# Optimization experiments

Measured on AMD Instinct MI355X. Metric: run time of the kernel, lower is better.

## Reference

```python
import jax, jax.numpy as jnp
import numpy as np

B, L, HID, H = 4, 1024, 1024, 16
D = HID // H  # 64

def setup_inputs() -> dict:
    key = jax.random.key(0)
    ks = jax.random.split(key, 9)
    s = 0.02
    return {
        'query_states': jax.random.normal(ks[0], (B, L, HID), jnp.float32),
        'key_states':   jax.random.normal(ks[1], (B, L, HID), jnp.float32),
        'value_states': jax.random.normal(ks[2], (B, L, HID), jnp.float32),
        'Wq': jax.random.normal(ks[3], (HID, HID), jnp.float32) * s,
        'bq': jnp.zeros((HID,), jnp.float32),
        'Wk': jax.random.normal(ks[4], (HID, HID), jnp.float32) * s,
        'bk': jnp.zeros((HID,), jnp.float32),
        'Wv': jax.random.normal(ks[5], (HID, HID), jnp.float32) * s,
        'bv': jnp.zeros((HID,), jnp.float32),
        'Wo': jax.random.normal(ks[6], (HID, HID), jnp.float32) * s,
        'bo': jnp.zeros((HID,), jnp.float32),
        'rel_pos_enc': jax.random.normal(ks[7], (2 * L - 1, D), jnp.float32),
    }

def _split_heads(x):
    # [B,L,HID] -> [B,H,L,D]
    return x.reshape(B, L, H, D).transpose(0, 2, 1, 3)

def reference(query_states, key_states, value_states, Wq, bq, Wk, bk, Wv, bv, Wo, bo, rel_pos_enc):
    q = _split_heads(query_states @ Wq + bq)  # [B,H,L,D]
    k = _split_heads(key_states @ Wk + bk)
    v = _split_heads(value_states @ Wv + bv)
    scores = jnp.einsum('bhld,bhrd->bhlr', q, k)
    # relative position bias
    pos = jnp.arange(L)
    distance = pos[:, None] - pos[None, :] + L - 1          # [L,L] in [0, 2L-2]
    pos_emb = rel_pos_enc[distance]                          # [L,L,D]
    scores = scores + jnp.einsum('bhld,lrd->bhlr', q, pos_emb)
    scores = scores / jnp.sqrt(jnp.asarray(D, scores.dtype))
    probs = jax.nn.softmax(scores, axis=-1)                  # dropout p=0 (eval)
    ctx = jnp.einsum('bhlr,bhrd->bhld', probs, v)
    ctx = ctx.transpose(0, 2, 1, 3).reshape(B, L, HID)
    out = ctx @ Wo + bo
    return (out, probs)
```

## Files before the change

### kernel.cpp

```cpp
#include <hip/hip_runtime.h>

typedef __bf16 bf16_t;
typedef bf16_t bf16x8 __attribute__((ext_vector_type(8)));
typedef bf16_t bf16x4 __attribute__((ext_vector_type(4)));
typedef float f32x16 __attribute__((ext_vector_type(16)));
typedef float f32x4v __attribute__((ext_vector_type(4)));
typedef unsigned int u32;

#define DEVI __device__ __forceinline__

DEVI f32x16 zero16() {
  f32x16 z;
#pragma unroll
  for (int i = 0; i < 16; ++i) z[i] = 0.0f;
  return z;
}

DEVI void gload16(const bf16_t* g, const unsigned short* l) {
  __builtin_amdgcn_global_load_lds(
      (const __attribute__((address_space(1))) u32*)g,
      (__attribute__((address_space(3))) u32*)l, 16, 0, 0);
}

union U16B { bf16x8 v; uint4 u; unsigned short s[8]; };
union U4B  { bf16_t h[4]; uint2 u; };

__global__ __launch_bounds__(256) void prep_kernel(
    const float* __restrict__ W0, const float* __restrict__ W1,
    const float* __restrict__ W2, const float* __restrict__ W3,
    bf16_t* __restrict__ T0, bf16_t* __restrict__ T1,
    bf16_t* __restrict__ T2, bf16_t* __restrict__ T3,
    const float* __restrict__ relE, bf16_t* __restrict__ Eb) {
  __shared__ float T[64][65];
  const int bid = blockIdx.x;
  const int tid = threadIdx.x;
  if (bid < 1024) {
    const int sel = bid >> 8;
    const float* W = sel == 0 ? W0 : sel == 1 ? W1 : sel == 2 ? W2 : W3;
    bf16_t* Wt = sel == 0 ? T0 : sel == 1 ? T1 : sel == 2 ? T2 : T3;
    const int bx = bid & 255;
    const int tx = bx & 15, ty = bx >> 4;
    const int k0 = ty * 64, n0 = tx * 64;
    {
      const int r = tid >> 4, c4 = (tid & 15) * 4;
#pragma unroll
      for (int rr = 0; rr < 64; rr += 16) {
        float4 v = *reinterpret_cast<const float4*>(&W[(size_t)(k0 + r + rr) * 1024 + n0 + c4]);
        T[r + rr][c4 + 0] = v.x; T[r + rr][c4 + 1] = v.y;
        T[r + rr][c4 + 2] = v.z; T[r + rr][c4 + 3] = v.w;
      }
    }
    __syncthreads();
    {
      const int r = tid >> 3, c8 = (tid & 7) * 8;
#pragma unroll
      for (int rr = 0; rr < 64; rr += 32) {
        U16B p;
#pragma unroll
        for (int i = 0; i < 8; ++i) p.v[i] = (bf16_t)T[c8 + i][r + rr];
        *reinterpret_cast<uint4*>(&Wt[(size_t)(n0 + r + rr) * 1024 + k0 + c8]) = p.u;
      }
    }
  } else {
    const int q = (bid - 1024) * 256 + tid;
    U4B p;
    if (q < 32752) {
      float4 v = *reinterpret_cast<const float4*>(&relE[(size_t)q * 4]);
      p.h[0] = (bf16_t)v.x; p.h[1] = (bf16_t)v.y; p.h[2] = (bf16_t)v.z; p.h[3] = (bf16_t)v.w;
    } else {
      p.h[0] = p.h[1] = p.h[2] = p.h[3] = (bf16_t)0.0f;
    }
    *reinterpret_cast<uint2*>(&Eb[(size_t)q * 4]) = p.u;
  }
}

#define ROWMAP(reg) (((reg) & 3) + 8 * ((reg) >> 2) + 4 * hi)

__global__ __launch_bounds__(512, 2) void gemm_qkv_kernel(
    const float* __restrict__ X0, const float* __restrict__ X1,
    const float* __restrict__ X2, const bf16_t* __restrict__ W0,
    const bf16_t* __restrict__ W1, const bf16_t* __restrict__ W2,
    const float* __restrict__ b0, const float* __restrict__ b1,
    const float* __restrict__ b2, bf16_t* __restrict__ O0,
    bf16_t* __restrict__ O1, bf16_t* __restrict__ O2) {
  __shared__ __align__(16) unsigned short As[2][256][64];
  __shared__ __align__(16) unsigned short Bs[2][256][64];
  const int f = blockIdx.x;
  const int fp = (f & 7) * 24 + (f >> 3);
  const int op = fp >> 6;
  const int r = fp & 63;
  const float* Xp = op == 0 ? X0 : op == 1 ? X1 : X2;
  const bf16_t* Wt = op == 0 ? W0 : op == 1 ? W1 : W2;
  const float* bias = op == 0 ? b0 : op == 1 ? b1 : b2;
  bf16_t* Out = op == 0 ? O0 : op == 1 ? O1 : O2;
  const int m0 = (r >> 2) * 256, n0 = (r & 3) * 256;
  const int tid = threadIdx.x;
  const int lane = tid & 63, wave = tid >> 6;
  const int hi = lane >> 5, ln = lane & 31;
  const int wr = wave >> 2, wc = wave & 3;
  const int srow = lane >> 3, scol = lane & 7;

  f32x16 acc[4][2];
#pragma unroll
  for (int rt = 0; rt < 4; ++rt) { acc[rt][0] = zero16(); acc[rt][1] = zero16(); }

  float4 fA[4][2];

#define ALOADR(kt)                                                                  \
  {                                                                                 \
    _Pragma("unroll")                                                               \
    for (int j = 0; j < 4; ++j) {                                                   \
      const int row = wave * 32 + j * 8 + srow;                                     \
      const float* src = &Xp[(size_t)(m0 + row) * 1024 + (kt) * 64 + scol * 8];     \
      fA[j][0] = *reinterpret_cast<const float4*>(src);                             \
      fA[j][1] = *reinterpret_cast<const float4*>(src + 4);                         \
    }                                                                               \
  }

#define ACVW(buf)                                                                   \
  {                                                                                 \
    _Pragma("unroll")                                                               \
    for (int j = 0; j < 4; ++j) {                                                   \
      const int row = wave * 32 + j * 8 + srow;                                     \
      U16B p;                                                                       \
      p.v[0] = (bf16_t)fA[j][0].x; p.v[1] = (bf16_t)fA[j][0].y;                     \
      p.v[2] = (bf16_t)fA[j][0].z; p.v[3] = (bf16_t)fA[j][0].w;                     \
      p.v[4] = (bf16_t)fA[j][1].x; p.v[5] = (bf16_t)fA[j][1].y;                     \
      p.v[6] = (bf16_t)fA[j][1].z; p.v[7] = (bf16_t)fA[j][1].w;                     \
      *reinterpret_cast<uint4*>(&As[buf][row][(scol ^ (row & 7)) * 8]) = p.u;       \
    }                                                                               \
  }

#define BGL(kt, buf)                                                                \
  {                                                                                 \
    _Pragma("unroll")                                                               \
    for (int j = 0; j < 4; ++j) {                                                   \
      const int rowbase = wave * 32 + j * 8;                                        \
      const int row = rowbase + srow;                                               \
      const int gc = scol ^ (row & 7);                                              \
      gload16(&Wt[(size_t)(n0 + row) * 1024 + (kt) * 64 + gc * 8],                  \
              &Bs[buf][rowbase][0]);                                                \
    }                                                                               \
  }

  ALOADR(0);
  asm volatile("s_waitcnt vmcnt(0)" ::: "memory");
  __builtin_amdgcn_sched_barrier(0);
  ACVW(0);
  BGL(0, 0);
  ALOADR(1);
  BGL(1, 1);

  for (int kt = 0; kt < 16; ++kt) {
    const int cur = kt & 1;
    if (kt < 15) {
      asm volatile("s_waitcnt vmcnt(12)" ::: "memory");
    } else {
      asm volatile("s_waitcnt vmcnt(0)" ::: "memory");
    }
    asm volatile("s_waitcnt lgkmcnt(0)" ::: "memory");
    __builtin_amdgcn_s_barrier();
    __builtin_amdgcn_sched_barrier(0);
#pragma unroll
    for (int kk = 0; kk < 4; ++kk) {
      const int ch = kk * 2 + hi;
      bf16x8 a[4], b[2];
#pragma unroll
      for (int rt = 0; rt < 4; ++rt) {
        const int ar = wr * 128 + rt * 32 + ln;
        a[rt] = *reinterpret_cast<const bf16x8*>(&As[cur][ar][(ch ^ (ar & 7)) * 8]);
      }
#pragma unroll
      for (int ct = 0; ct < 2; ++ct) {
        const int br = wc * 64 + ct * 32 + ln;
        b[ct] = *reinterpret_cast<const bf16x8*>(&Bs[cur][br][(ch ^ (br & 7)) * 8]);
      }
#pragma unroll
      for (int rt = 0; rt < 4; ++rt)
#pragma unroll
        for (int ct = 0; ct < 2; ++ct)
          acc[rt][ct] = __builtin_amdgcn_mfma_f32_32x32x16_bf16(a[rt], b[ct], acc[rt][ct], 0, 0, 0);
    }
    __builtin_amdgcn_sched_barrier(0);
    if (kt + 1 < 16) {
      asm volatile("s_waitcnt vmcnt(4)" ::: "memory");
      __builtin_amdgcn_sched_barrier(0);
      ACVW(cur ^ 1);
      if (kt + 2 < 16) ALOADR(kt + 2);
    }
    asm volatile("s_waitcnt lgkmcnt(0)" ::: "memory");
    __builtin_amdgcn_s_barrier();
    __builtin_amdgcn_sched_barrier(0);
    if (kt + 2 < 16) BGL(kt + 2, cur);
  }
#undef ALOADR
#undef ACVW
#undef BGL

#pragma unroll
  for (int ct = 0; ct < 2; ++ct) {
    const int nc = n0 + wc * 64 + ct * 32 + ln;
    const float bv = bias[nc];
    const int h = nc >> 6, d = nc & 63;
    if (op < 2) {
#pragma unroll
      for (int rt = 0; rt < 4; ++rt)
#pragma unroll
        for (int reg = 0; reg < 16; ++reg) {
          const int mr = m0 + wr * 128 + rt * 32 + ROWMAP(reg);
          const int b = mr >> 10, l = mr & 1023;
          Out[(((size_t)(b * 16 + h)) * 1024 + l) * 64 + d] =
              (bf16_t)(acc[rt][ct][reg] + bv);
        }
    } else {
#pragma unroll
      for (int rt = 0; rt < 4; ++rt)
#pragma unroll
        for (int g = 0; g < 4; ++g) {
          const int l4 = m0 + wr * 128 + rt * 32 + g * 8 + 4 * hi;
          const int b = l4 >> 10, ll = l4 & 1023;
          U4B p;
#pragma unroll
          for (int j = 0; j < 4; ++j) p.h[j] = (bf16_t)(acc[rt][ct][g * 4 + j] + bv);
          *reinterpret_cast<uint2*>(
              &Out[(((size_t)(b * 16 + h)) * 64 + d) * 1024 + ll]) = p.u;
        }
    }
  }
}

__global__ __launch_bounds__(256) void gemm_o_kernel(
    const bf16_t* __restrict__ A0, const bf16_t* __restrict__ W0,
    const float* __restrict__ b0, float* __restrict__ O0) {
  __shared__ __align__(16) unsigned short As[2][128][64];
  __shared__ __align__(16) unsigned short Bs[2][128][64];
  const int f = blockIdx.x;
  const int fp = (f & 7) * 32 + (f >> 3);
  const int r = fp;
  const int m0 = (r >> 3) * 128, n0 = (r & 7) * 128;
  const int tid = threadIdx.x;
  const int lane = tid & 63, wave = tid >> 6;
  const int hi = lane >> 5, ln = lane & 31;
  const int wr = wave >> 1, wc = wave & 1;
  const int srow = lane >> 3, scol = lane & 7;

  f32x16 acc[2][2];
  acc[0][0] = zero16(); acc[0][1] = zero16();
  acc[1][0] = zero16(); acc[1][1] = zero16();

#define STAGE_O(kt, buf)                                                            \
  {                                                                                 \
    _Pragma("unroll")                                                               \
    for (int j = 0; j < 4; ++j) {                                                   \
      const int rowbase = wave * 32 + j * 8;                                        \
      const int row = rowbase + srow;                                               \
      const int gc = scol ^ (row & 7);                                              \
      gload16(&A0[(size_t)(m0 + row) * 1024 + (kt) * 64 + gc * 8],                  \
              &As[buf][rowbase][0]);                                                \
      gload16(&W0[(size_t)(n0 + row) * 1024 + (kt) * 64 + gc * 8],                  \
              &Bs[buf][rowbase][0]);                                                \
    }                                                                               \
  }

  STAGE_O(0, 0);
  STAGE_O(1, 1);

  for (int kt = 0; kt < 16; ++kt) {
    const int cur = kt & 1;
    if (kt < 15) {
      asm volatile("s_waitcnt vmcnt(8)" ::: "memory");
    } else {
      asm volatile("s_waitcnt vmcnt(0)" ::: "memory");
    }
    __builtin_amdgcn_s_barrier();
    __builtin_amdgcn_sched_barrier(0);
#pragma unroll
    for (int kk = 0; kk < 4; ++kk) {
      const int ch = kk * 2 + hi;
      const int ar0 = wr * 64 + ln, ar1 = ar0 + 32;
      const int br0 = wc * 64 + ln, br1 = br0 + 32;
      bf16x8 a0 = *reinterpret_cast<const bf16x8*>(&As[cur][ar0][(ch ^ (ar0 & 7)) * 8]);
      bf16x8 a1 = *reinterpret_cast<const bf16x8*>(&As[cur][ar1][(ch ^ (ar1 & 7)) * 8]);
      bf16x8 bb0 = *reinterpret_cast<const bf16x8*>(&Bs[cur][br0][(ch ^ (br0 & 7)) * 8]);
      bf16x8 bb1 = *reinterpret_cast<const bf16x8*>(&Bs[cur][br1][(ch ^ (br1 & 7)) * 8]);
      acc[0][0] = __builtin_amdgcn_mfma_f32_32x32x16_bf16(a0, bb0, acc[0][0], 0, 0, 0);
      acc[0][1] = __builtin_amdgcn_mfma_f32_32x32x16_bf16(a0, bb1, acc[0][1], 0, 0, 0);
      acc[1][0] = __builtin_amdgcn_mfma_f32_32x32x16_bf16(a1, bb0, acc[1][0], 0, 0, 0);
      acc[1][1] = __builtin_amdgcn_mfma_f32_32x32x16_bf16(a1, bb1, acc[1][1], 0, 0, 0);
    }
    __builtin_amdgcn_sched_barrier(0);
    __builtin_amdgcn_s_barrier();
    __builtin_amdgcn_sched_barrier(0);
    if (kt + 2 < 16) STAGE_O(kt + 2, cur);
  }
#undef STAGE_O

#pragma unroll
  for (int cb = 0; cb < 2; ++cb) {
    const int nc = n0 + wc * 64 + cb * 32 + ln;
    const float bv = b0[nc];
#pragma unroll
    for (int rb = 0; rb < 2; ++rb)
#pragma unroll
      for (int reg = 0; reg < 16; ++reg) {
        const int mr = m0 + wr * 64 + rb * 32 + ROWMAP(reg);
        O0[(size_t)mr * 1024 + nc] = acc[rb][cb][reg] + bv;
      }
  }
}

__global__ __launch_bounds__(512, 4) void attn_kernel(
    const bf16_t* __restrict__ q, const bf16_t* __restrict__ k,
    const bf16_t* __restrict__ vt, const bf16_t* __restrict__ E,
    float* __restrict__ probs, bf16_t* __restrict__ ctx) {
  __shared__ __align__(16) unsigned short Pbuf[8][32][128];
  __shared__ float rstat[32][9];
  const int f = blockIdx.x;
  const int fp = (f & 7) * 256 + (f >> 3);
  const int bh = fp >> 5;
  const int l0 = (fp & 31) * 32;
  const int tid = threadIdx.x;
  const int lane = tid & 63, wave = tid >> 6;
  const int hi = lane >> 5, ln = lane & 31;
  const bf16_t* qb = q + (size_t)bh * 1024 * 64;
  const bf16_t* kb = k + (size_t)bh * 1024 * 64;
  const bf16_t* vb = vt + (size_t)bh * 64 * 1024;
  const int rbase = wave * 128;
  const int b0 = l0 - rbase + 992;

  bf16x8 qf[4];
#pragma unroll
  for (int kk = 0; kk < 4; ++kk)
    qf[kk] = *reinterpret_cast<const bf16x8*>(&qb[(size_t)(l0 + ln) * 64 + kk * 16 + hi * 8]);

  f32x16 tpre = zero16();
  __builtin_amdgcn_s_setprio(1);
#pragma unroll
  for (int kk = 0; kk < 4; ++kk) {
    bf16x8 e = *reinterpret_cast<const bf16x8*>(
        &E[(size_t)(b0 + 32 + ln) * 64 + kk * 16 + hi * 8]);
    tpre = __builtin_amdgcn_mfma_f32_32x32x16_bf16(qf[kk], e, tpre, 0, 0, 0);
  }
  __builtin_amdgcn_s_setprio(0);

#pragma unroll
  for (int t = 0; t < 4; ++t) {
    const int r0 = rbase + t * 32;
    f32x16 acc = zero16();
    f32x16 tcur = zero16();
    __builtin_amdgcn_s_setprio(1);
#pragma unroll
    for (int kk = 0; kk < 4; ++kk) {
      bf16x8 kf = *reinterpret_cast<const bf16x8*>(
          &kb[(size_t)(r0 + ln) * 64 + kk * 16 + hi * 8]);
      acc = __builtin_amdgcn_mfma_f32_32x32x16_bf16(qf[kk], kf, acc, 0, 0, 0);
      bf16x8 e = *reinterpret_cast<const bf16x8*>(
          &E[(size_t)(b0 - 32 * t + ln) * 64 + kk * 16 + hi * 8]);
      tcur = __builtin_amdgcn_mfma_f32_32x32x16_bf16(qf[kk], e, tcur, 0, 0, 0);
    }
    __builtin_amdgcn_s_setprio(0);
#pragma unroll
    for (int reg = 0; reg < 16; ++reg) {
      const int i = ROWMAP(reg);
      const int w = i - ln + 31;
      const int src = (w & 31) + (hi << 5);
      acc[reg] += __shfl((ln >= i) ? tcur[reg] : tpre[reg], src, 64);
    }
    const int col = t * 32 + ln;
#pragma unroll
    for (int reg = 0; reg < 16; ++reg) {
      const int i = ROWMAP(reg);
      union { bf16_t h; unsigned short u; } cv;
      cv.h = (bf16_t)exp2f(acc[reg] * 0.1803368801f);
      Pbuf[wave][i][((col >> 3) ^ (i & 7)) * 8 + (col & 7)] = cv.u;
    }
    tpre = tcur;
  }

  {
    float s = 0.0f;
#pragma unroll
    for (int g = 0; g < 8; ++g) {
      const int cg = hi * 8 + g;
      bf16x8 pv = *reinterpret_cast<const bf16x8*>(
          &Pbuf[wave][ln][((cg ^ (ln & 7))) * 8]);
#pragma unroll
      for (int e = 0; e < 8; ++e) s += (float)pv[e];
    }
    s += __shfl_xor(s, 32, 64);
    if (hi == 0) rstat[ln][wave] = s;
  }

  f32x16 pv0 = zero16(), pv1 = zero16();
  __builtin_amdgcn_s_setprio(1);
#pragma unroll
  for (int kk = 0; kk < 8; ++kk) {
    const int ch = kk * 2 + hi;
    bf16x8 pa = *reinterpret_cast<const bf16x8*>(&Pbuf[wave][ln][(ch ^ (ln & 7)) * 8]);
    bf16x8 v0 = *reinterpret_cast<const bf16x8*>(
        &vb[(size_t)ln * 1024 + rbase + kk * 16 + hi * 8]);
    bf16x8 v1 = *reinterpret_cast<const bf16x8*>(
        &vb[(size_t)(32 + ln) * 1024 + rbase + kk * 16 + hi * 8]);
    pv0 = __builtin_amdgcn_mfma_f32_32x32x16_bf16(pa, v0, pv0, 0, 0, 0);
    pv1 = __builtin_amdgcn_mfma_f32_32x32x16_bf16(pa, v1, pv1, 0, 0, 0);
  }
  __builtin_amdgcn_s_setprio(0);

  __syncthreads();

  float inv;
  {
    float s = 0.0f;
#pragma unroll
    for (int w = 0; w < 8; ++w) s += rstat[ln][w];
    inv = 1.0f / s;
  }

  float* pb = probs + ((size_t)bh * 1024 + l0) * 1024;
#pragma unroll
  for (int it = 0; it < 16; ++it) {
    const int r = it * 2 + hi;
    const float invr = __shfl(inv, r, 64);
    const int g = ln >> 1;
    bf16x4 pv = *reinterpret_cast<const bf16x4*>(
        &Pbuf[wave][r][(g ^ (r & 7)) * 8 + (ln & 1) * 4]);
    f32x4v o;
    o[0] = (float)pv[0] * invr; o[1] = (float)pv[1] * invr;
    o[2] = (float)pv[2] * invr; o[3] = (float)pv[3] * invr;
    __builtin_nontemporal_store(
        o, reinterpret_cast<f32x4v*>(&pb[(size_t)r * 1024 + rbase + ln * 4]));
  }

  float* cred = reinterpret_cast<float*>(&Pbuf[0][0][0]);
  if (wave < 4) {
#pragma unroll
    for (int reg = 0; reg < 16; ++reg) {
      const int i = ROWMAP(reg);
      cred[((size_t)wave * 32 + i) * 64 + ln] = pv0[reg];
      cred[((size_t)wave * 32 + i) * 64 + 32 + ln] = pv1[reg];
    }
  }
  __syncthreads();
  if (wave >= 4) {
    const int s = wave - 4;
#pragma unroll
    for (int reg = 0; reg < 16; ++reg) {
      const int i = ROWMAP(reg);
      cred[((size_t)s * 32 + i) * 64 + ln] += pv0[reg];
      cred[((size_t)s * 32 + i) * 64 + 32 + ln] += pv1[reg];
    }
  }
  __syncthreads();
  {
    const int i = tid >> 4, d0 = (tid & 15) * 4;
    float4 a = *reinterpret_cast<const float4*>(&cred[(size_t)(0 * 32 + i) * 64 + d0]);
#pragma unroll
    for (int s = 1; s < 4; ++s) {
      float4 b = *reinterpret_cast<const float4*>(&cred[(size_t)(s * 32 + i) * 64 + d0]);
      a.x += b.x; a.y += b.y; a.z += b.z; a.w += b.w;
    }
    const float invr = __shfl(inv, i, 64);
    U4B o;
    o.h[0] = (bf16_t)(a.x * invr); o.h[1] = (bf16_t)(a.y * invr);
    o.h[2] = (bf16_t)(a.z * invr); o.h[3] = (bf16_t)(a.w * invr);
    const int b = bh >> 4, h = bh & 15;
    *reinterpret_cast<uint2*>(&ctx[((((size_t)b * 1024) + l0 + i) * 16 + h) * 64 + d0]) = o.u;
  }
}

extern "C" void kernel_launch(void* const* d_in, const int* in_sizes, int n_in,
                              void* d_out, int out_size, void* d_ws, size_t ws_size,
                              hipStream_t stream) {
  const float* xq = (const float*)d_in[0];
  const float* xk = (const float*)d_in[1];
  const float* xv = (const float*)d_in[2];
  const float* Wq = (const float*)d_in[3];
  const float* bq = (const float*)d_in[4];
  const float* Wk = (const float*)d_in[5];
  const float* bk = (const float*)d_in[6];
  const float* Wv = (const float*)d_in[7];
  const float* bv = (const float*)d_in[8];
  const float* Wo = (const float*)d_in[9];
  const float* bo = (const float*)d_in[10];
  const float* relE = (const float*)d_in[11];

  char* ws = (char*)d_ws;
  const size_t MB2 = 1u << 21;
  bf16_t* WtQ = (bf16_t*)(ws + 0 * MB2);
  bf16_t* WtK = (bf16_t*)(ws + 1 * MB2);
  bf16_t* WtV = (bf16_t*)(ws + 2 * MB2);
  bf16_t* WtO = (bf16_t*)(ws + 3 * MB2);
  bf16_t* Eb  = (bf16_t*)(ws + 4 * MB2);
  bf16_t* qb  = (bf16_t*)(ws + 4 * MB2 + (1u << 19));
  bf16_t* kb  = qb + (size_t)4 * 16 * 1024 * 64;
  bf16_t* vtb = kb + (size_t)4 * 16 * 1024 * 64;
  bf16_t* ctxb = vtb + (size_t)4 * 16 * 1024 * 64;

  float* outp = (float*)d_out;
  float* probs = outp + (size_t)4 * 1024 * 1024;

  prep_kernel<<<1152, 256, 0, stream>>>(Wq, Wk, Wv, Wo, WtQ, WtK, WtV, WtO,
                                        relE, Eb);
  gemm_qkv_kernel<<<192, 512, 0, stream>>>(xq, xk, xv, WtQ, WtK, WtV,
                                           bq, bk, bv, qb, kb, vtb);
  attn_kernel<<<2048, 512, 0, stream>>>(qb, kb, vtb, Eb, probs, ctxb);
  gemm_o_kernel<<<256, 256, 0, stream>>>(ctxb, WtO, bo, outp);
}
```

Measured before the change: 190.8 us.

## Retile attention to 16-row blocks with 16 waves using 16x16 MFMA

The attention kernel now handles 16 query rows per block with 1024 threads (16 waves, each owning 64 key columns) instead of 32 rows with 8 waves, using 16x16x32 MFMA tiles. The probability strip and the cross-wave context reduction share one LDS buffer, and the probs store is done straight from registers loaded earlier. The intent is more parallelism and shorter per-wave dependency chains. The cost is twice as many blocks, each reloading K, V and E with less reuse per block, plus a larger 16-way LDS reduction, and launch_bounds(1024,8) may put pressure on registers.

```diff
diff --git a/kernel.cpp b/kernel.cpp
--- a/kernel.cpp
+++ b/kernel.cpp
@@ -309,162 +309,153 @@
   }
 }
 
-__global__ __launch_bounds__(512, 4) void attn_kernel(
+__global__ __launch_bounds__(1024, 8) void attn_kernel(
     const bf16_t* __restrict__ q, const bf16_t* __restrict__ k,
     const bf16_t* __restrict__ vt, const bf16_t* __restrict__ E,
     float* __restrict__ probs, bf16_t* __restrict__ ctx) {
-  __shared__ __align__(16) unsigned short Pbuf[8][32][128];
-  __shared__ float rstat[32][9];
+  __shared__ __align__(16) float cred[16][16][64];
+  __shared__ float rstat[16][17];
+  unsigned short* strip = reinterpret_cast<unsigned short*>(&cred[0][0][0]);
   const int f = blockIdx.x;
-  const int fp = (f & 7) * 256 + (f >> 3);
-  const int bh = fp >> 5;
-  const int l0 = (fp & 31) * 32;
+  const int fp = (f & 7) * 512 + (f >> 3);
+  const int bh = fp >> 6;
+  const int l0 = (fp & 63) * 16;
   const int tid = threadIdx.x;
-  const int lane = tid & 63, wave = tid >> 6;
-  const int hi = lane >> 5, ln = lane & 31;
+  const int lane = tid & 63, wv = tid >> 6;
+  const int lr = lane & 15;
+  const int lg = lane >> 4;
   const bf16_t* qb = q + (size_t)bh * 1024 * 64;
   const bf16_t* kb = k + (size_t)bh * 1024 * 64;
   const bf16_t* vb = vt + (size_t)bh * 64 * 1024;
-  const int rbase = wave * 128;
-  const int b0 = l0 - rbase + 992;
-
-  bf16x8 qf[4];
-#pragma unroll
-  for (int kk = 0; kk < 4; ++kk)
-    qf[kk] = *reinterpret_cast<const bf16x8*>(&qb[(size_t)(l0 + ln) * 64 + kk * 16 + hi * 8]);
-
-  f32x16 tpre = zero16();
-  __builtin_amdgcn_s_setprio(1);
-#pragma unroll
-  for (int kk = 0; kk < 4; ++kk) {
-    bf16x8 e = *reinterpret_cast<const bf16x8*>(
-        &E[(size_t)(b0 + 32 + ln) * 64 + kk * 16 + hi * 8]);
-    tpre = __builtin_amdgcn_mfma_f32_32x32x16_bf16(qf[kk], e, tpre, 0, 0, 0);
-  }
-  __builtin_amdgcn_s_setprio(0);
+  const int c0 = wv * 64;
+  const int eb0 = l0 - c0 + 1008;
+
+  bf16x8 qf0 = *reinterpret_cast<const bf16x8*>(&qb[(size_t)(l0 + lr) * 64 + lg * 8]);
+  bf16x8 qf1 = *reinterpret_cast<const bf16x8*>(&qb[(size_t)(l0 + lr) * 64 + 32 + lg * 8]);
+
+  f32x4v tpre = {0.0f, 0.0f, 0.0f, 0.0f};
+  {
+    bf16x8 e0 = *reinterpret_cast<const bf16x8*>(&E[(size_t)(eb0 + 16 + lr) * 64 + lg * 8]);
+    bf16x8 e1 = *reinterpret_cast<const bf16x8*>(&E[(size_t)(eb0 + 16 + lr) * 64 + 32 + lg * 8]);
+    tpre = __builtin_amdgcn_mfma_f32_16x16x32_bf16(qf0, e0, tpre, 0, 0, 0);
+    tpre = __builtin_amdgcn_mfma_f32_16x16x32_bf16(qf1, e1, tpre, 0, 0, 0);
+  }
 
 #pragma unroll
   for (int t = 0; t < 4; ++t) {
-    const int r0 = rbase + t * 32;
-    f32x16 acc = zero16();
-    f32x16 tcur = zero16();
+    const int r0 = c0 + 16 * t;
+    const int eb = eb0 - 16 * t;
+    f32x4v acc = {0.0f, 0.0f, 0.0f, 0.0f};
+    f32x4v tcur = {0.0f, 0.0f, 0.0f, 0.0f};
     __builtin_amdgcn_s_setprio(1);
-#pragma unroll
-    for (int kk = 0; kk < 4; ++kk) {
-      bf16x8 kf = *reinterpret_cast<const bf16x8*>(
-          &kb[(size_t)(r0 + ln) * 64 + kk * 16 + hi * 8]);
-      acc = __builtin_amdgcn_mfma_f32_32x32x16_bf16(qf[kk], kf, acc, 0, 0, 0);
-      bf16x8 e = *reinterpret_cast<const bf16x8*>(
-          &E[(size_t)(b0 - 32 * t + ln) * 64 + kk * 16 + hi * 8]);
-      tcur = __builtin_amdgcn_mfma_f32_32x32x16_bf16(qf[kk], e, tcur, 0, 0, 0);
+    {
+      bf16x8 kf0 = *reinterpret_cast<const bf16x8*>(&kb[(size_t)(r0 + lr) * 64 + lg * 8]);
+      bf16x8 kf1 = *reinterpret_cast<const bf16x8*>(&kb[(size_t)(r0 + lr) * 64 + 32 + lg * 8]);
+      acc = __builtin_amdgcn_mfma_f32_16x16x32_bf16(qf0, kf0, acc, 0, 0, 0);
+      acc = __builtin_amdgcn_mfma_f32_16x16x32_bf16(qf1, kf1, acc, 0, 0, 0);
+      bf16x8 e0 = *reinterpret_cast<const bf16x8*>(&E[(size_t)(eb + lr) * 64 + lg * 8]);
+      bf16x8 e1 = *reinterpret_cast<const bf16x8*>(&E[(size_t)(eb + lr) * 64 + 32 + lg * 8]);
+      tcur = __builtin_amdgcn_mfma_f32_16x16x32_bf16(qf0, e0, tcur, 0, 0, 0);
+      tcur = __builtin_amdgcn_mfma_f32_16x16x32_bf16(qf1, e1, tcur, 0, 0, 0);
     }
     __builtin_amdgcn_s_setprio(0);
 #pragma unroll
-    for (int reg = 0; reg < 16; ++reg) {
-      const int i = ROWMAP(reg);
-      const int w = i - ln + 31;
-      const int src = (w & 31) + (hi << 5);
-      acc[reg] += __shfl((ln >= i) ? tcur[reg] : tpre[reg], src, 64);
-    }
-    const int col = t * 32 + ln;
-#pragma unroll
-    for (int reg = 0; reg < 16; ++reg) {
-      const int i = ROWMAP(reg);
+    for (int reg = 0; reg < 4; ++reg) {
+      const int l = lg * 4 + reg;
+      const int src = (lane & 48) | ((l - lr + 15) & 15);
+      const float sel = (lr >= l) ? tcur[reg] : tpre[reg];
+      const float sv = acc[reg] + __shfl(sel, src, 64);
       union { bf16_t h; unsigned short u; } cv;
-      cv.h = (bf16_t)exp2f(acc[reg] * 0.1803368801f);
-      Pbuf[wave][i][((col >> 3) ^ (i & 7)) * 8 + (col & 7)] = cv.u;
+      cv.h = (bf16_t)exp2f(sv * 0.1803368801f);
+      const int colg = r0 + lr;
+      strip[(size_t)l * 1024 + (colg ^ ((l & 7) << 3))] = cv.u;
     }
     tpre = tcur;
   }
 
-  {
+  bf16x8 pr0, pr1;
+  float inv;
+  {
+    const int ch0 = (8 * wv + 2 * lg + 0) ^ (lr & 7);
+    const int ch1 = (8 * wv + 2 * lg + 1) ^ (lr & 7);
+    pr0 = *reinterpret_cast<const bf16x8*>(&strip[(size_t)lr * 1024 + ch0 * 8]);
+    pr1 = *reinterpret_cast<const bf16x8*>(&strip[(size_t)lr * 1024 + ch1 * 8]);
     float s = 0.0f;
 #pragma unroll
-    for (int g = 0; g < 8; ++g) {
-      const int cg = hi * 8 + g;
-      bf16x8 pv = *reinterpret_cast<const bf16x8*>(
-          &Pbuf[wave][ln][((cg ^ (ln & 7))) * 8]);
-#pragma unroll
-      for (int e = 0; e < 8; ++e) s += (float)pv[e];
-    }
+    for (int e = 0; e < 8; ++e) s += (float)pr0[e] + (float)pr1[e];
+    s += __shfl_xor(s, 16, 64);
     s += __shfl_xor(s, 32, 64);
-    if (hi == 0) rstat[ln][wave] = s;
-  }
-
-  f32x16 pv0 = zero16(), pv1 = zero16();
-  __builtin_amdgcn_s_setprio(1);
-#pragma unroll
-  for (int kk = 0; kk < 8; ++kk) {
-    const int ch = kk * 2 + hi;
-    bf16x8 pa = *reinterpret_cast<const bf16x8*>(&Pbuf[wave][ln][(ch ^ (ln & 7)) * 8]);
-    bf16x8 v0 = *reinterpret_cast<const bf16x8*>(
-        &vb[(size_t)ln * 1024 + rbase + kk * 16 + hi * 8]);
-    bf16x8 v1 = *reinterpret_cast<const bf16x8*>(
-        &vb[(size_t)(32 + ln) * 1024 + rbase + kk * 16 + hi * 8]);
-    pv0 = __builtin_amdgcn_mfma_f32_32x32x16_bf16(pa, v0, pv0, 0, 0, 0);
-    pv1 = __builtin_amdgcn_mfma_f32_32x32x16_bf16(pa, v1, pv1, 0, 0, 0);
-  }
-  __builtin_amdgcn_s_setprio(0);
+    if (lane < 16) rstat[lr][wv] = s;
+  }
+
+  f32x4v pv0 = {0,0,0,0}, pv1 = {0,0,0,0}, pv2 = {0,0,0,0}, pv3 = {0,0,0,0};
+  {
+    const int cha = (8 * wv + 0 * 4 + lg) ^ (lr & 7);
+    const int chb = (8 * wv + 1 * 4 + lg) ^ (lr & 7);
+    bf16x8 pa0 = *reinterpret_cast<const bf16x8*>(&strip[(size_t)lr * 1024 + cha * 8]);
+    bf16x8 pa1 = *reinterpret_cast<const bf16x8*>(&strip[(size_t)lr * 1024 + chb * 8]);
+    __builtin_amdgcn_s_setprio(1);
+#pragma unroll
+    for (int dt = 0; dt < 4; ++dt) {
+      bf16x8 v0 = *reinterpret_cast<const bf16x8*>(
+          &vb[(size_t)(dt * 16 + lr) * 1024 + c0 + lg * 8]);
+      bf16x8 v1 = *reinterpret_cast<const bf16x8*>(
+          &vb[(size_t)(dt * 16 + lr) * 1024 + c0 + 32 + lg * 8]);
+      f32x4v* pvp = dt == 0 ? &pv0 : dt == 1 ? &pv1 : dt == 2 ? &pv2 : &pv3;
+      *pvp = __builtin_amdgcn_mfma_f32_16x16x32_bf16(pa0, v0, *pvp, 0, 0, 0);
+      *pvp = __builtin_amdgcn_mfma_f32_16x16x32_bf16(pa1, v1, *pvp, 0, 0, 0);
+    }
+    __builtin_amdgcn_s_setprio(0);
+  }
 
   __syncthreads();
 
-  float inv;
   {
     float s = 0.0f;
 #pragma unroll
-    for (int w = 0; w < 8; ++w) s += rstat[ln][w];
+    for (int w = 0; w < 16; ++w) s += rstat[lr][w];
     inv = 1.0f / s;
   }
 
-  float* pb = probs + ((size_t)bh * 1024 + l0) * 1024;
-#pragma unroll
-  for (int it = 0; it < 16; ++it) {
-    const int r = it * 2 + hi;
-    const float invr = __shfl(inv, r, 64);
-    const int g = ln >> 1;
-    bf16x4 pv = *reinterpret_cast<const bf16x4*>(
-        &Pbuf[wave][r][(g ^ (r & 7)) * 8 + (ln & 1) * 4]);
+#pragma unroll
+  for (int reg = 0; reg < 4; ++reg) {
+    const int row = lg * 4 + reg;
+    cred[wv][row][0 * 16 + lr] = pv0[reg];
+    cred[wv][row][1 * 16 + lr] = pv1[reg];
+    cred[wv][row][2 * 16 + lr] = pv2[reg];
+    cred[wv][row][3 * 16 + lr] = pv3[reg];
+  }
+  __syncthreads();
+
+  {
+    const int row = tid >> 6, d = tid & 63;
+    float a = 0.0f;
+#pragma unroll
+    for (int s16 = 0; s16 < 16; ++s16) a += cred[s16][row][d];
+    float rs = 0.0f;
+#pragma unroll
+    for (int w = 0; w < 16; ++w) rs += rstat[row][w];
+    const int b = bh >> 4, h = bh & 15;
+    ctx[((((size_t)b * 1024) + l0 + row) * 16 + h) * 64 + d] = (bf16_t)(a / rs);
+  }
+
+  {
+    float* pb = probs + ((size_t)bh * 1024 + l0) * 1024 + (size_t)lr * 1024;
+    const int tc0 = (8 * wv + 2 * lg + 0) * 8;
+    const int tc1 = (8 * wv + 2 * lg + 1) * 8;
     f32x4v o;
-    o[0] = (float)pv[0] * invr; o[1] = (float)pv[1] * invr;
-    o[2] = (float)pv[2] * invr; o[3] = (float)pv[3] * invr;
-    __builtin_nontemporal_store(
-        o, reinterpret_cast<f32x4v*>(&pb[(size_t)r * 1024 + rbase + ln * 4]));
-  }
-
-  float* cred = reinterpret_cast<float*>(&Pbuf[0][0][0]);
-  if (wave < 4) {
-#pragma unroll
-    for (int reg = 0; reg < 16; ++reg) {
-      const int i = ROWMAP(reg);
-      cred[((size_t)wave * 32 + i) * 64 + ln] = pv0[reg];
-      cred[((size_t)wave * 32 + i) * 64 + 32 + ln] = pv1[reg];
-    }
-  }
-  __syncthreads();
-  if (wave >= 4) {
-    const int s = wave - 4;
-#pragma unroll
-    for (int reg = 0; reg < 16; ++reg) {
-      const int i = ROWMAP(reg);
-      cred[((size_t)s * 32 + i) * 64 + ln] += pv0[reg];
-      cred[((size_t)s * 32 + i) * 64 + 32 + ln] += pv1[reg];
-    }
-  }
-  __syncthreads();
-  {
-    const int i = tid >> 4, d0 = (tid & 15) * 4;
-    float4 a = *reinterpret_cast<const float4*>(&cred[(size_t)(0 * 32 + i) * 64 + d0]);
-#pragma unroll
-    for (int s = 1; s < 4; ++s) {
-      float4 b = *reinterpret_cast<const float4*>(&cred[(size_t)(s * 32 + i) * 64 + d0]);
-      a.x += b.x; a.y += b.y; a.z += b.z; a.w += b.w;
-    }
-    const float invr = __shfl(inv, i, 64);
-    U4B o;
-    o.h[0] = (bf16_t)(a.x * invr); o.h[1] = (bf16_t)(a.y * invr);
-    o.h[2] = (bf16_t)(a.z * invr); o.h[3] = (bf16_t)(a.w * invr);
-    const int b = bh >> 4, h = bh & 15;
-    *reinterpret_cast<uint2*>(&ctx[((((size_t)b * 1024) + l0 + i) * 16 + h) * 64 + d0]) = o.u;
+    o[0] = (float)pr0[0] * inv; o[1] = (float)pr0[1] * inv;
+    o[2] = (float)pr0[2] * inv; o[3] = (float)pr0[3] * inv;
+    __builtin_nontemporal_store(o, reinterpret_cast<f32x4v*>(&pb[tc0]));
+    o[0] = (float)pr0[4] * inv; o[1] = (float)pr0[5] * inv;
+    o[2] = (float)pr0[6] * inv; o[3] = (float)pr0[7] * inv;
+    __builtin_nontemporal_store(o, reinterpret_cast<f32x4v*>(&pb[tc0 + 4]));
+    o[0] = (float)pr1[0] * inv; o[1] = (float)pr1[1] * inv;
+    o[2] = (float)pr1[2] * inv; o[3] = (float)pr1[3] * inv;
+    __builtin_nontemporal_store(o, reinterpret_cast<f32x4v*>(&pb[tc1]));
+    o[0] = (float)pr1[4] * inv; o[1] = (float)pr1[5] * inv;
+    o[2] = (float)pr1[6] * inv; o[3] = (float)pr1[7] * inv;
+    __builtin_nontemporal_store(o, reinterpret_cast<f32x4v*>(&pb[tc1 + 4]));
   }
 }
 
@@ -503,6 +494,6 @@
                                         relE, Eb);
   gemm_qkv_kernel<<<192, 512, 0, stream>>>(xq, xk, xv, WtQ, WtK, WtV,
                                            bq, bk, bv, qb, kb, vtb);
-  attn_kernel<<<2048, 512, 0, stream>>>(qb, kb, vtb, Eb, probs, ctxb);
+  attn_kernel<<<4096, 1024, 0, stream>>>(qb, kb, vtb, Eb, probs, ctxb);
   gemm_o_kernel<<<256, 256, 0, stream>>>(ctxb, WtO, bo, outp);
 }
```

After: 482.8 us. 153% more time.
